# Optimization experiments

Measured on AMD Instinct MI355X. Metric: run time of the kernel, lower is better.

Reference implementation:

```python
import jax, jax.numpy as jnp
import numpy as np

D_MODEL, H, D_FF = 1024, 16, 4096
D_K = D_MODEL // H
EPS = 1e-5


def _layernorm(x, alpha, bias):
    # faithful to source: unbiased std (ddof=1), eps added to std (not var)
    mean = jnp.mean(x, axis=-1, keepdims=True)
    std = jnp.std(x, axis=-1, keepdims=True, ddof=1)
    return alpha * (x - mean) / (std + EPS) + bias


def setup_inputs() -> dict:
    key = jax.random.key(0)
    ks = jax.random.split(key, 12)
    B, S = 2, 2048
    s = 1.0 / np.sqrt(D_MODEL)
    inp = {
        "x": jax.random.normal(ks[0], (B, S, D_MODEL), dtype=jnp.float32),
        "mask": jnp.ones((B, 1, 1, S), dtype=jnp.int32),
        "wq": jax.random.normal(ks[1], (D_MODEL, D_MODEL), dtype=jnp.float32) * s,
        "wk": jax.random.normal(ks[2], (D_MODEL, D_MODEL), dtype=jnp.float32) * s,
        "wv": jax.random.normal(ks[3], (D_MODEL, D_MODEL), dtype=jnp.float32) * s,
        "wo": jax.random.normal(ks[4], (D_MODEL, D_MODEL), dtype=jnp.float32) * s,
        "w1": jax.random.normal(ks[5], (D_MODEL, D_FF), dtype=jnp.float32) * s,
        "b1": jnp.zeros((D_FF,), dtype=jnp.float32),
        "w2": jax.random.normal(ks[6], (D_FF, D_MODEL), dtype=jnp.float32) * (1.0 / np.sqrt(D_FF)),
        "b2": jnp.zeros((D_MODEL,), dtype=jnp.float32),
        "alpha1": jnp.ones((1,), dtype=jnp.float32),
        "bias1": jnp.zeros((1,), dtype=jnp.float32),
        "alpha2": jnp.ones((1,), dtype=jnp.float32),
        "bias2": jnp.zeros((1,), dtype=jnp.float32),
    }
    return inp


def reference(x, mask, wq, wk, wv, wo, w1, b1, w2, b2, alpha1, bias1, alpha2, bias2):
    B, S, _ = x.shape

    # --- sublayer 1: pre-norm self-attention + residual ---
    xn = _layernorm(x, alpha1, bias1)
    q = (xn @ wq).reshape(B, S, H, D_K).transpose(0, 2, 1, 3)  # [B,H,S,Dk]
    k = (xn @ wk).reshape(B, S, H, D_K).transpose(0, 2, 1, 3)
    v = (xn @ wv).reshape(B, S, H, D_K).transpose(0, 2, 1, 3)

    scores = jnp.einsum("bhqd,bhkd->bhqk", q, k) / np.sqrt(D_K)  # [B,H,S,S]
    scores = jnp.where(mask == 0, jnp.float32(-1e9), scores)
    attn = jax.nn.softmax(scores, axis=-1)
    ctx = jnp.einsum("bhqk,bhkd->bhqd", attn, v)
    ctx = ctx.transpose(0, 2, 1, 3).reshape(B, S, D_MODEL)
    x = x + ctx @ wo

    # --- sublayer 2: pre-norm FFN + residual ---
    xn = _layernorm(x, alpha2, bias2)
    h = jax.nn.relu(xn @ w1 + b1)
    x = x + h @ w2 + b2
    return x
```

## Files before the change

### kernel.cpp

```cpp
#include <hip/hip_runtime.h>
#include <hip/hip_bf16.h>

typedef __attribute__((ext_vector_type(8))) short bf16x8;
typedef __attribute__((ext_vector_type(4))) short short4v;
typedef __attribute__((ext_vector_type(4))) float floatx4;

#define MFMA16(A, B, C) __builtin_amdgcn_mfma_f32_16x16x32_bf16((A), (B), (C), 0, 0, 0)

__device__ inline short bf16bits(float f) {
  __hip_bfloat16 h = __float2bfloat16(f);
  return *reinterpret_cast<short*>(&h);
}
__device__ inline unsigned cvtpk(float lo, float hi) {
  unsigned r;
  asm("v_cvt_pk_bf16_f32 %0, %1, %2" : "=v"(r) : "v"(lo), "v"(hi));
  return r;
}
typedef __attribute__((address_space(3))) char lds_char;
typedef __attribute__((address_space(1))) const char glob_char;
__device__ inline void gll16(const void* g, void* l) {
  __builtin_amdgcn_global_load_lds((glob_char*)g, (lds_char*)l, 16, 0, 0);
}

__global__ __launch_bounds__(256) void transpose_f2b_kernel(
    const float* __restrict__ src, __hip_bfloat16* __restrict__ dst,
    int R, int C, int ldS) {
  __shared__ __align__(16) __hip_bfloat16 tile[64][72];
  const long r0 = (long)blockIdx.y * 64, c0 = (long)blockIdx.x * 64;
  for (int i = threadIdx.x; i < 1024; i += 256) {
    int r = i >> 4, c4 = (i & 15) * 4;
    float4 f = *(const float4*)&src[(r0 + r) * ldS + c0 + c4];
    short4v s;
    s[0] = bf16bits(f.x); s[1] = bf16bits(f.y);
    s[2] = bf16bits(f.z); s[3] = bf16bits(f.w);
    *(short4v*)&tile[r][c4] = s;
  }
  __syncthreads();
  for (int i = threadIdx.x; i < 512; i += 256) {
    int c = i >> 3, r8 = (i & 7) * 8;
    bf16x8 sv;
#pragma unroll
    for (int j = 0; j < 8; j++) sv[j] = *reinterpret_cast<const short*>(&tile[r8 + j][c]);
    *(bf16x8*)&dst[(c0 + c) * R + r0 + r8] = sv;
  }
}

__global__ __launch_bounds__(256) void transpose_qkv_kernel(
    const float* __restrict__ wq, const float* __restrict__ wk,
    const float* __restrict__ wv, __hip_bfloat16* __restrict__ wqkvT) {
  __shared__ __align__(16) __hip_bfloat16 tile[64][72];
  const int which = blockIdx.y >> 4;
  const float* src = which == 0 ? wq : (which == 1 ? wk : wv);
  __hip_bfloat16* dst = wqkvT + (size_t)which * 1024 * 1024;
  const long r0 = (long)(blockIdx.y & 15) * 64, c0 = (long)blockIdx.x * 64;
  for (int i = threadIdx.x; i < 1024; i += 256) {
    int r = i >> 4, c4 = (i & 15) * 4;
    float4 f = *(const float4*)&src[(r0 + r) * 1024 + c0 + c4];
    short4v s;
    s[0] = bf16bits(f.x); s[1] = bf16bits(f.y);
    s[2] = bf16bits(f.z); s[3] = bf16bits(f.w);
    *(short4v*)&tile[r][c4] = s;
  }
  __syncthreads();
  for (int i = threadIdx.x; i < 512; i += 256) {
    int c = i >> 3, r8 = (i & 7) * 8;
    bf16x8 sv;
#pragma unroll
    for (int j = 0; j < 8; j++) sv[j] = *reinterpret_cast<const short*>(&tile[r8 + j][c]);
    *(bf16x8*)&dst[(c0 + c) * 1024 + r0 + r8] = sv;
  }
}

__global__ __launch_bounds__(256) void vtrans_kernel(
    const __hip_bfloat16* __restrict__ qkv, __hip_bfloat16* __restrict__ vt) {
  __shared__ __align__(16) __hip_bfloat16 tile[64][72];
  const int bh = blockIdx.y, b = bh >> 4, h = bh & 15;
  const long s0 = (long)blockIdx.x * 64;
  const __hip_bfloat16* src = qkv + ((long)b * 2048 + s0) * 3072 + 2048 + h * 64;
  for (int i = threadIdx.x; i < 512; i += 256) {
    int s = i >> 3, d8 = (i & 7) * 8;
    *(uint4*)&tile[s][d8] = *(const uint4*)&src[(long)s * 3072 + d8];
  }
  __syncthreads();
  __hip_bfloat16* dstb = vt + (long)bh * 64 * 2048 + s0;
  for (int i = threadIdx.x; i < 512; i += 256) {
    int d = i >> 3, s8 = (i & 7) * 8;
    bf16x8 sv;
#pragma unroll
    for (int j = 0; j < 8; j++) sv[j] = *reinterpret_cast<const short*>(&tile[s8 + j][d]);
    *(bf16x8*)&dstb[(long)d * 2048 + s8] = sv;
  }
}

__global__ __launch_bounds__(256) void mask2add_kernel(
    const int* __restrict__ mask, float* __restrict__ addm,
    int* __restrict__ flags) {
  const int i = blockIdx.x * 256 + threadIdx.x;
  const int mv = mask[i];
  addm[i] = mv ? 0.f : -1e30f;
  __shared__ int ok[4];
  const unsigned long long bal = __ballot(mv != 0);
  if ((threadIdx.x & 63) == 0) ok[threadIdx.x >> 6] = (bal == ~0ull) ? 1 : 0;
  __syncthreads();
  if (threadIdx.x == 0) flags[blockIdx.x] = ok[0] & ok[1] & ok[2] & ok[3];
}

__global__ __launch_bounds__(256) void bias_add_kernel(
    const float* __restrict__ x1, const float* __restrict__ b2,
    float* __restrict__ out) {
  const int i = (blockIdx.x * 256 + threadIdx.x) * 4;
  float4 v = *(const float4*)&x1[i];
  const float4 bb = *(const float4*)&b2[i & 1023];
  v.x += bb.x; v.y += bb.y; v.z += bb.z; v.w += bb.w;
  *(float4*)&out[i] = v;
}

__global__ __launch_bounds__(256) void ln_kernel(
    const float* __restrict__ x, __hip_bfloat16* __restrict__ y,
    const float* __restrict__ alpha_p, const float* __restrict__ bias_p) {
  __shared__ float sred[8];
  const long row = blockIdx.x;
  const int t = threadIdx.x;
  const float* xr = x + row * 1024;
  float v[4];
#pragma unroll
  for (int i = 0; i < 4; i++) v[i] = xr[t * 4 + i];
  float sum = 0.f, sq = 0.f;
#pragma unroll
  for (int i = 0; i < 4; i++) { sum += v[i]; sq += v[i] * v[i]; }
#pragma unroll
  for (int off = 32; off; off >>= 1) {
    sum += __shfl_down(sum, off);
    sq += __shfl_down(sq, off);
  }
  if ((t & 63) == 0) { sred[(t >> 6) * 2] = sum; sred[(t >> 6) * 2 + 1] = sq; }
  __syncthreads();
  sum = sred[0] + sred[2] + sred[4] + sred[6];
  sq = sred[1] + sred[3] + sred[5] + sred[7];
  const float mean = sum * (1.f / 1024.f);
  float var = (sq - 1024.f * mean * mean) * (1.f / 1023.f);
  var = fmaxf(var, 0.f);
  const float denom = sqrtf(var) + 1e-5f;
  const float sc = alpha_p[0] / denom;
  const float beta = bias_p[0];
  __hip_bfloat16* yr = y + row * 1024;
#pragma unroll
  for (int i = 0; i < 4; i++) yr[t * 4 + i] = __float2bfloat16((v[i] - mean) * sc + beta);
}

template <int EPI>
__global__ __launch_bounds__(256) void gemm_bt_kernel(
    const __hip_bfloat16* __restrict__ A, const __hip_bfloat16* __restrict__ Bt,
    void* __restrict__ Cv, const float* __restrict__ bias,
    const float* __restrict__ res, int M, int N, int K) {
  __shared__ __align__(16) __hip_bfloat16 lA[2][128 * 32];
  __shared__ __align__(16) __hip_bfloat16 lB[2][128 * 32];
  const int tid = threadIdx.x;
  const int wave = tid >> 6, lane = tid & 63;
  const int quad = lane >> 4, l16 = lane & 15;
  const int wm = wave >> 1, wn = wave & 1;

  const int gx = gridDim.x;
  const int nwg = gx * gridDim.y;
  int bid = blockIdx.y * gx + blockIdx.x;
  bid = (bid & 7) * (nwg >> 3) + (bid >> 3);
  const long m0 = (long)(bid / gx) * 128;
  const long n0 = (long)(bid % gx) * 128;

  const int rA0 = tid >> 2, cA0 = (tid & 3) * 8;
  const int rA1 = (tid + 256) >> 2, cA1 = ((tid + 256) & 3) * 8;

  floatx4 acc[4][4];
#pragma unroll
  for (int i = 0; i < 4; i++)
#pragma unroll
    for (int j = 0; j < 4; j++) acc[i][j] = (floatx4){0.f, 0.f, 0.f, 0.f};

  const __hip_bfloat16* Ab = A + m0 * K;
  const __hip_bfloat16* Bb = Bt + n0 * K;

  gll16(&Ab[(long)rA0 * K + cA0], &lA[0][wave * 512]);
  gll16(&Ab[(long)rA1 * K + cA1], &lA[0][2048 + wave * 512]);
  gll16(&Bb[(long)rA0 * K + cA0], &lB[0][wave * 512]);
  gll16(&Bb[(long)rA1 * K + cA1], &lB[0][2048 + wave * 512]);

  int cur = 0;
  for (int k0 = 0; k0 < K; k0 += 32) {
    __syncthreads();
    if (k0 + 32 < K) {
      const int nxt = cur ^ 1;
      gll16(&Ab[(long)rA0 * K + k0 + 32 + cA0], &lA[nxt][wave * 512]);
      gll16(&Ab[(long)rA1 * K + k0 + 32 + cA1], &lA[nxt][2048 + wave * 512]);
      gll16(&Bb[(long)rA0 * K + k0 + 32 + cA0], &lB[nxt][wave * 512]);
      gll16(&Bb[(long)rA1 * K + k0 + 32 + cA1], &lB[nxt][2048 + wave * 512]);
    }
    bf16x8 af[4], bfr[4];
#pragma unroll
    for (int mi = 0; mi < 4; mi++)
      af[mi] = *(const bf16x8*)&lA[cur][(wm * 64 + mi * 16 + l16) * 32 + quad * 8];
#pragma unroll
    for (int ni = 0; ni < 4; ni++)
      bfr[ni] = *(const bf16x8*)&lB[cur][(wn * 64 + ni * 16 + l16) * 32 + quad * 8];
#pragma unroll
    for (int mi = 0; mi < 4; mi++)
#pragma unroll
      for (int ni = 0; ni < 4; ni++)
        acc[mi][ni] = MFMA16(af[mi], bfr[ni], acc[mi][ni]);
    cur ^= 1;
  }

#pragma unroll
  for (int mi = 0; mi < 4; mi++) {
#pragma unroll
    for (int ni = 0; ni < 4; ni++) {
#pragma unroll
      for (int r = 0; r < 4; r++) {
        const long row = m0 + wm * 64 + mi * 16 + quad * 4 + r;
        const long col = n0 + wn * 64 + ni * 16 + l16;
        const long idx = row * N + col;
        float v = acc[mi][ni][r];
        if (EPI == 0) {
          ((__hip_bfloat16*)Cv)[idx] = __float2bfloat16(v);
        } else if (EPI == 1) {
          ((float*)Cv)[idx] = v + res[idx];
        } else if (EPI == 2) {
          v += bias[col];
          ((__hip_bfloat16*)Cv)[idx] = __float2bfloat16(fmaxf(v, 0.f));
        } else if (EPI == 3) {
          float* Cf = (float*)Cv;
          Cf[idx] = Cf[idx] + v;
        }
      }
    }
  }
}

template <int EPI>
__global__ __launch_bounds__(256) void gemm64_bt_kernel(
    const __hip_bfloat16* __restrict__ A, const __hip_bfloat16* __restrict__ Bt,
    void* __restrict__ Cv, const float* __restrict__ bias,
    const float* __restrict__ res, int M, int N, int K) {
  __shared__ __align__(16) __hip_bfloat16 lA[2][128 * 32];
  __shared__ __align__(16) __hip_bfloat16 lB[2][64 * 32];
  const int tid = threadIdx.x;
  const int wave = tid >> 6, lane = tid & 63;
  const int quad = lane >> 4, l16 = lane & 15;
  const int wm = wave >> 1, wn = wave & 1;

  const int gx = gridDim.x;
  const int nwg = gx * gridDim.y;
  int bid = blockIdx.y * gx + blockIdx.x;
  bid = (bid & 7) * (nwg >> 3) + (bid >> 3);
  const long m0 = (long)(bid / gx) * 128;
  const long n0 = (long)(bid % gx) * 64;

  const int rA0 = tid >> 2, cA0 = (tid & 3) * 8;
  const int rA1 = (tid + 256) >> 2, cA1 = ((tid + 256) & 3) * 8;

  floatx4 acc[4][2];
#pragma unroll
  for (int i = 0; i < 4; i++)
#pragma unroll
    for (int j = 0; j < 2; j++) acc[i][j] = (floatx4){0.f, 0.f, 0.f, 0.f};

  const __hip_bfloat16* Ab = A + m0 * K;
  const __hip_bfloat16* Bb = Bt + n0 * K;

  gll16(&Ab[(long)rA0 * K + cA0], &lA[0][wave * 512]);
  gll16(&Ab[(long)rA1 * K + cA1], &lA[0][2048 + wave * 512]);
  gll16(&Bb[(long)rA0 * K + cA0], &lB[0][wave * 512]);

  int cur = 0;
  for (int k0 = 0; k0 < K; k0 += 32) {
    __syncthreads();
    if (k0 + 32 < K) {
      const int nxt = cur ^ 1;
      gll16(&Ab[(long)rA0 * K + k0 + 32 + cA0], &lA[nxt][wave * 512]);
      gll16(&Ab[(long)rA1 * K + k0 + 32 + cA1], &lA[nxt][2048 + wave * 512]);
      gll16(&Bb[(long)rA0 * K + k0 + 32 + cA0], &lB[nxt][wave * 512]);
    }
    bf16x8 af[4], bfr[2];
#pragma unroll
    for (int mi = 0; mi < 4; mi++)
      af[mi] = *(const bf16x8*)&lA[cur][(wm * 64 + mi * 16 + l16) * 32 + quad * 8];
#pragma unroll
    for (int ni = 0; ni < 2; ni++)
      bfr[ni] = *(const bf16x8*)&lB[cur][(wn * 32 + ni * 16 + l16) * 32 + quad * 8];
#pragma unroll
    for (int mi = 0; mi < 4; mi++)
#pragma unroll
      for (int ni = 0; ni < 2; ni++)
        acc[mi][ni] = MFMA16(af[mi], bfr[ni], acc[mi][ni]);
    cur ^= 1;
  }

#pragma unroll
  for (int mi = 0; mi < 4; mi++) {
#pragma unroll
    for (int ni = 0; ni < 2; ni++) {
#pragma unroll
      for (int r = 0; r < 4; r++) {
        const long row = m0 + wm * 64 + mi * 16 + quad * 4 + r;
        const long col = n0 + wn * 32 + ni * 16 + l16;
        const long idx = row * N + col;
        float v = acc[mi][ni][r];
        if (EPI == 1) {
          ((float*)Cv)[idx] = v + res[idx];
        } else if (EPI == 3) {
          float* Cf = (float*)Cv;
          Cf[idx] = Cf[idx] + v;
        }
      }
    }
  }
}

__global__ __launch_bounds__(256) void attn_kernel(
    const __hip_bfloat16* __restrict__ qkv, const __hip_bfloat16* __restrict__ vt,
    const float* __restrict__ addm, const int* __restrict__ flags,
    __hip_bfloat16* __restrict__ ctx) {
  __shared__ __align__(16) __hip_bfloat16 lK[2][64 * 64];
  __shared__ __align__(16) __hip_bfloat16 lV[2][64 * 64];
  const int tid = threadIdx.x, wave = tid >> 6, lane = tid & 63;
  const int quad = lane >> 4, l16 = lane & 15;
  const int bh = blockIdx.y, b = bh >> 4, h = bh & 15;
  const int q0 = blockIdx.x * 64 + wave * 16;
  const float cs = 0.18033688011112042f;
  const float inv_cs = 5.545177444479562f;

  const __hip_bfloat16* kb = qkv + (long)b * 2048 * 3072 + 1024 + h * 64;
  const __hip_bfloat16* vb = vt + (long)bh * 64 * 2048;
  const float* am = addm + b * 2048;

  int fm = 1;
#pragma unroll
  for (int i = 0; i < 8; ++i) fm &= flags[b * 8 + i];
  const bool fast = (fm != 0);

  const long qoff = ((long)b * 2048 + q0 + l16) * 3072 + h * 64;
  const bf16x8 bq0 = *(const bf16x8*)&qkv[qoff + quad * 8];
  const bf16x8 bq1 = *(const bf16x8*)&qkv[qoff + 32 + quad * 8];

  const int srow = lane >> 3;
  const int cslot = lane & 7;
  const int cg = cslot ^ srow;
  const int rbase = wave * 16 + srow;

  floatx4 o[4];
#pragma unroll
  for (int mi = 0; mi < 4; mi++) o[mi] = (floatx4){0.f, 0.f, 0.f, 0.f};
  float mrow = 10.0f, lrow = 0.f;

#pragma unroll
  for (int j = 0; j < 2; ++j) {
    const int rloc = rbase + j * 8;
    gll16(kb + (long)rloc * 3072 + cg * 8, &lK[0][(wave * 16 + j * 8) * 64]);
    gll16(vb + (long)rloc * 2048 + cg * 8, &lV[0][(wave * 16 + j * 8) * 64]);
  }

  int cur = 0;
  for (int t = 0; t < 32; ++t) {
    __syncthreads();
    if (t + 1 < 32) {
      const int nxt = cur ^ 1;
#pragma unroll
      for (int j = 0; j < 2; ++j) {
        const int rloc = rbase + j * 8;
        gll16(kb + (long)((t + 1) * 64 + rloc) * 3072 + cg * 8,
              &lK[nxt][(wave * 16 + j * 8) * 64]);
        gll16(vb + (long)rloc * 2048 + (t + 1) * 64 + cg * 8,
              &lV[nxt][(wave * 16 + j * 8) * 64]);
      }
    }
    const __hip_bfloat16* lKc = lK[cur];
    const __hip_bfloat16* lVc = lV[cur];

    floatx4 c[4];
    __builtin_amdgcn_s_setprio(1);
#pragma unroll
    for (int g = 0; g < 4; ++g) {
      const bf16x8 a0 =
          *(const bf16x8*)&lKc[(g * 16 + l16) * 64 + ((quad) ^ (l16 & 7)) * 8];
      const bf16x8 a1 =
          *(const bf16x8*)&lKc[(g * 16 + l16) * 64 + ((4 + quad) ^ (l16 & 7)) * 8];
      floatx4 cc = {0.f, 0.f, 0.f, 0.f};
      cc = MFMA16(a0, bq0, cc);
      cc = MFMA16(a1, bq1, cc);
      c[g] = cc;
    }
    __builtin_amdgcn_s_setprio(0);

    if (!fast) {
#pragma unroll
      for (int g = 0; g < 4; ++g) {
        const float4 a4 = *(const float4*)&am[t * 64 + g * 16 + quad * 4];
        c[g][0] = fmaf(a4.x, inv_cs, c[g][0]);
        c[g][1] = fmaf(a4.y, inv_cs, c[g][1]);
        c[g][2] = fmaf(a4.z, inv_cs, c[g][2]);
        c[g][3] = fmaf(a4.w, inv_cs, c[g][3]);
      }
    }

    const float mneg = -mrow;
    float p[4][4];
#pragma unroll
    for (int g = 0; g < 4; ++g)
#pragma unroll
      for (int r = 0; r < 4; ++r)
        p[g][r] = __builtin_amdgcn_exp2f(fmaf(c[g][r], cs, mneg));

    const float m0 = fmaxf(fmaxf(c[0][0], c[0][1]), c[0][2]);
    const float m1 = fmaxf(fmaxf(c[0][3], c[1][0]), c[1][1]);
    const float m2 = fmaxf(fmaxf(c[1][2], c[1][3]), c[2][0]);
    const float m3 = fmaxf(fmaxf(c[2][1], c[2][2]), c[2][3]);
    const float m4 = fmaxf(fmaxf(c[3][0], c[3][1]), c[3][2]);
    float tm = fmaxf(fmaxf(fmaxf(m0, m1), fmaxf(m2, m3)), fmaxf(m4, c[3][3]));
    tm = fmaxf(tm, __shfl_xor(tm, 16));
    tm = fmaxf(tm, __shfl_xor(tm, 32));
    const float tms = tm * cs;

    const float s0 = (p[0][0] + p[0][1]) + (p[0][2] + p[0][3]);
    const float s1 = (p[1][0] + p[1][1]) + (p[1][2] + p[1][3]);
    const float s2 = (p[2][0] + p[2][1]) + (p[2][2] + p[2][3]);
    const float s3 = (p[3][0] + p[3][1]) + (p[3][2] + p[3][3]);
    float rs = (s0 + s1) + (s2 + s3);
    rs += __shfl_xor(rs, 16);
    rs += __shfl_xor(rs, 32);

    unsigned dw[4][2];
#pragma unroll
    for (int g = 0; g < 4; ++g) {
      dw[g][0] = cvtpk(p[g][0], p[g][1]);
      dw[g][1] = cvtpk(p[g][2], p[g][3]);
    }
    const int qs0 = (quad & 1) * 2;
    const int src0 = l16 + 16 * qs0, src1 = src0 + 16;
    const bool hig = (quad >> 1) != 0;
#pragma unroll
    for (int ss = 0; ss < 2; ++ss) {
      const unsigned a0 = __shfl((int)dw[2 * ss][0], src0);
      const unsigned b0 = __shfl((int)dw[2 * ss + 1][0], src0);
      const unsigned a1 = __shfl((int)dw[2 * ss][1], src0);
      const unsigned b1 = __shfl((int)dw[2 * ss + 1][1], src0);
      const unsigned a2 = __shfl((int)dw[2 * ss][0], src1);
      const unsigned b2 = __shfl((int)dw[2 * ss + 1][0], src1);
      const unsigned a3 = __shfl((int)dw[2 * ss][1], src1);
      const unsigned b3 = __shfl((int)dw[2 * ss + 1][1], src1);
      uint4 du;
      du.x = hig ? b0 : a0;
      du.y = hig ? b1 : a1;
      du.z = hig ? b2 : a2;
      du.w = hig ? b3 : a3;
      const bf16x8 bp = *reinterpret_cast<bf16x8*>(&du);
      __builtin_amdgcn_s_setprio(1);
#pragma unroll
      for (int mi = 0; mi < 4; ++mi) {
        const bf16x8 av = *(const bf16x8*)&lVc[(mi * 16 + l16) * 64 +
                                               ((ss * 4 + quad) ^ (l16 & 7)) * 8];
        o[mi] = MFMA16(av, bp, o[mi]);
      }
      __builtin_amdgcn_s_setprio(0);
    }

    lrow += rs;
    if (__any(tms > mrow + 8.f)) {
      const float mnew = fmaxf(mrow, tms);
      const float alpha = __builtin_amdgcn_exp2f(mrow - mnew);
      mrow = mnew;
      lrow *= alpha;
#pragma unroll
      for (int mi = 0; mi < 4; mi++) o[mi] *= alpha;
    }
    cur ^= 1;
  }

  const float inv_l = 1.f / lrow;
  const long cb = ((long)b * 2048 + q0 + l16) * 1024 + h * 64;
#pragma unroll
  for (int mi = 0; mi < 4; mi++) {
    uint2 st;
    st.x = cvtpk(o[mi][0] * inv_l, o[mi][1] * inv_l);
    st.y = cvtpk(o[mi][2] * inv_l, o[mi][3] * inv_l);
    *(uint2*)&ctx[cb + mi * 16 + quad * 4] = st;
  }
}

extern "C" void kernel_launch(void* const* d_in, const int* in_sizes, int n_in,
                              void* d_out, int out_size, void* d_ws, size_t ws_size,
                              hipStream_t stream) {
  const float* x = (const float*)d_in[0];
  const int* mask = (const int*)d_in[1];
  const float* wq = (const float*)d_in[2];
  const float* wk = (const float*)d_in[3];
  const float* wv = (const float*)d_in[4];
  const float* wo = (const float*)d_in[5];
  const float* w1 = (const float*)d_in[6];
  const float* b1 = (const float*)d_in[7];
  const float* w2 = (const float*)d_in[8];
  const float* b2 = (const float*)d_in[9];
  const float* alpha1 = (const float*)d_in[10];
  const float* bias1 = (const float*)d_in[11];
  const float* alpha2 = (const float*)d_in[12];
  const float* bias2 = (const float*)d_in[13];

  char* ws = (char*)d_ws;
  char* dob = (char*)d_out;
  const size_t MiB = 1048576;
  __hip_bfloat16* qkv   = (__hip_bfloat16*)(ws + 0);
  __hip_bfloat16* wqkvT = (__hip_bfloat16*)(ws + 24 * MiB);
  __hip_bfloat16* vtb   = (__hip_bfloat16*)(ws + 24 * MiB);
  float*          x1    = (float*)(ws + 0);
  __hip_bfloat16* hc    = (__hip_bfloat16*)(ws + 16 * MiB);
  __hip_bfloat16* xn    = (__hip_bfloat16*)d_out;
  __hip_bfloat16* ctxb  = (__hip_bfloat16*)d_out;
  __hip_bfloat16* xn2   = (__hip_bfloat16*)d_out;
  __hip_bfloat16* woT   = (__hip_bfloat16*)(dob + 8 * MiB);
  __hip_bfloat16* w1Th  = (__hip_bfloat16*)(dob + 8 * MiB);
  __hip_bfloat16* w2Th  = (__hip_bfloat16*)(dob + 12 * MiB);
  float*          addm  = (float*)(dob + 12 * MiB);
  int*            flags = (int*)(dob + 12 * MiB + 16 * 1024);

  const dim3 b256(256);
  const dim3 g1k(16, 16);
  transpose_qkv_kernel<<<dim3(16, 48), b256, 0, stream>>>(wq, wk, wv, wqkvT);
  ln_kernel<<<4096, b256, 0, stream>>>(x, xn, alpha1, bias1);
  gemm_bt_kernel<0><<<dim3(24, 32), b256, 0, stream>>>(xn, wqkvT, qkv, nullptr, nullptr,
                                                       4096, 3072, 1024);
  vtrans_kernel<<<dim3(32, 32), b256, 0, stream>>>(qkv, vtb);
  mask2add_kernel<<<16, b256, 0, stream>>>(mask, addm, flags);
  attn_kernel<<<dim3(32, 32), b256, 0, stream>>>(qkv, vtb, addm, flags, ctxb);
  transpose_f2b_kernel<<<g1k, b256, 0, stream>>>(wo, woT, 1024, 1024, 1024);
  gemm64_bt_kernel<1><<<dim3(16, 32), b256, 0, stream>>>(ctxb, woT, x1, nullptr, x,
                                                         4096, 1024, 1024);
  ln_kernel<<<4096, b256, 0, stream>>>(x1, xn2, alpha2, bias2);
  for (int c = 0; c < 2; ++c) {
    transpose_f2b_kernel<<<dim3(32, 16), b256, 0, stream>>>(w1 + c * 2048, w1Th,
                                                            1024, 2048, 4096);
    gemm_bt_kernel<2><<<dim3(16, 32), b256, 0, stream>>>(xn2, w1Th, hc, b1 + c * 2048,
                                                         nullptr, 4096, 2048, 1024);
    transpose_f2b_kernel<<<dim3(16, 32), b256, 0, stream>>>(w2 + (size_t)c * 2048 * 1024,
                                                            w2Th, 2048, 1024, 1024);
    gemm64_bt_kernel<3><<<dim3(16, 32), b256, 0, stream>>>(hc, w2Th, x1, nullptr,
                                                           nullptr, 4096, 1024, 2048);
  }
  bias_add_kernel<<<4096, b256, 0, stream>>>(x1, b2, (float*)d_out);
}
```

Baseline: 438.2 us.

## Deepen gemm64 K-tile to 64 with XOR-swizzled LDS and merge prep launches

The 128x64 GEMM used for the Wo and W2 projections now stages 64-wide K slices instead of 32. It stores them in LDS with an XOR swizzle on the 16-byte chunk index, which halves the number of barrier-separated iterations and aims to avoid LDS bank conflicts on fragment reads. The V transpose, Wo transpose and mask conversion are merged into one prep kernel, and the W1 and W2 per-chunk transposes are merged into one wtrans kernel, cutting several small launches. The larger tiles double LDS use per block, which may lower occupancy.

```diff
diff --git a/kernel.cpp b/kernel.cpp
--- a/kernel.cpp
+++ b/kernel.cpp
@@ -20,29 +20,6 @@
 typedef __attribute__((address_space(1))) const char glob_char;
 __device__ inline void gll16(const void* g, void* l) {
   __builtin_amdgcn_global_load_lds((glob_char*)g, (lds_char*)l, 16, 0, 0);
-}
-
-__global__ __launch_bounds__(256) void transpose_f2b_kernel(
-    const float* __restrict__ src, __hip_bfloat16* __restrict__ dst,
-    int R, int C, int ldS) {
-  __shared__ __align__(16) __hip_bfloat16 tile[64][72];
-  const long r0 = (long)blockIdx.y * 64, c0 = (long)blockIdx.x * 64;
-  for (int i = threadIdx.x; i < 1024; i += 256) {
-    int r = i >> 4, c4 = (i & 15) * 4;
-    float4 f = *(const float4*)&src[(r0 + r) * ldS + c0 + c4];
-    short4v s;
-    s[0] = bf16bits(f.x); s[1] = bf16bits(f.y);
-    s[2] = bf16bits(f.z); s[3] = bf16bits(f.w);
-    *(short4v*)&tile[r][c4] = s;
-  }
-  __syncthreads();
-  for (int i = threadIdx.x; i < 512; i += 256) {
-    int c = i >> 3, r8 = (i & 7) * 8;
-    bf16x8 sv;
-#pragma unroll
-    for (int j = 0; j < 8; j++) sv[j] = *reinterpret_cast<const short*>(&tile[r8 + j][c]);
-    *(bf16x8*)&dst[(c0 + c) * R + r0 + r8] = sv;
-  }
 }
 
 __global__ __launch_bounds__(256) void transpose_qkv_kernel(
@@ -71,38 +48,94 @@
   }
 }
 
-__global__ __launch_bounds__(256) void vtrans_kernel(
-    const __hip_bfloat16* __restrict__ qkv, __hip_bfloat16* __restrict__ vt) {
-  __shared__ __align__(16) __hip_bfloat16 tile[64][72];
-  const int bh = blockIdx.y, b = bh >> 4, h = bh & 15;
-  const long s0 = (long)blockIdx.x * 64;
-  const __hip_bfloat16* src = qkv + ((long)b * 2048 + s0) * 3072 + 2048 + h * 64;
-  for (int i = threadIdx.x; i < 512; i += 256) {
-    int s = i >> 3, d8 = (i & 7) * 8;
-    *(uint4*)&tile[s][d8] = *(const uint4*)&src[(long)s * 3072 + d8];
-  }
-  __syncthreads();
-  __hip_bfloat16* dstb = vt + (long)bh * 64 * 2048 + s0;
-  for (int i = threadIdx.x; i < 512; i += 256) {
-    int d = i >> 3, s8 = (i & 7) * 8;
-    bf16x8 sv;
-#pragma unroll
-    for (int j = 0; j < 8; j++) sv[j] = *reinterpret_cast<const short*>(&tile[s8 + j][d]);
-    *(bf16x8*)&dstb[(long)d * 2048 + s8] = sv;
-  }
-}
-
-__global__ __launch_bounds__(256) void mask2add_kernel(
+__global__ __launch_bounds__(256) void prep_kernel(
+    const __hip_bfloat16* __restrict__ qkv, __hip_bfloat16* __restrict__ vt,
+    const float* __restrict__ wo, __hip_bfloat16* __restrict__ woT,
     const int* __restrict__ mask, float* __restrict__ addm,
     int* __restrict__ flags) {
-  const int i = blockIdx.x * 256 + threadIdx.x;
-  const int mv = mask[i];
-  addm[i] = mv ? 0.f : -1e30f;
+  __shared__ __align__(16) __hip_bfloat16 tile[64][72];
   __shared__ int ok[4];
-  const unsigned long long bal = __ballot(mv != 0);
-  if ((threadIdx.x & 63) == 0) ok[threadIdx.x >> 6] = (bal == ~0ull) ? 1 : 0;
+  const int bid = blockIdx.x;
+  if (bid < 1024) {
+    const int bh = bid >> 5, b = bh >> 4, h = bh & 15;
+    const long s0 = (long)(bid & 31) * 64;
+    const __hip_bfloat16* src = qkv + ((long)b * 2048 + s0) * 3072 + 2048 + h * 64;
+    for (int i = threadIdx.x; i < 512; i += 256) {
+      int s = i >> 3, d8 = (i & 7) * 8;
+      *(uint4*)&tile[s][d8] = *(const uint4*)&src[(long)s * 3072 + d8];
+    }
+    __syncthreads();
+    __hip_bfloat16* dstb = vt + (long)bh * 64 * 2048 + s0;
+    for (int i = threadIdx.x; i < 512; i += 256) {
+      int d = i >> 3, s8 = (i & 7) * 8;
+      bf16x8 sv;
+#pragma unroll
+      for (int j = 0; j < 8; j++) sv[j] = *reinterpret_cast<const short*>(&tile[s8 + j][d]);
+      *(bf16x8*)&dstb[(long)d * 2048 + s8] = sv;
+    }
+  } else if (bid < 1280) {
+    const int t = bid - 1024;
+    const long r0 = (long)(t >> 4) * 64, c0 = (long)(t & 15) * 64;
+    for (int i = threadIdx.x; i < 1024; i += 256) {
+      int r = i >> 4, c4 = (i & 15) * 4;
+      float4 f = *(const float4*)&wo[(r0 + r) * 1024 + c0 + c4];
+      short4v s;
+      s[0] = bf16bits(f.x); s[1] = bf16bits(f.y);
+      s[2] = bf16bits(f.z); s[3] = bf16bits(f.w);
+      *(short4v*)&tile[r][c4] = s;
+    }
+    __syncthreads();
+    for (int i = threadIdx.x; i < 512; i += 256) {
+      int c = i >> 3, r8 = (i & 7) * 8;
+      bf16x8 sv;
+#pragma unroll
+      for (int j = 0; j < 8; j++) sv[j] = *reinterpret_cast<const short*>(&tile[r8 + j][c]);
+      *(bf16x8*)&woT[(c0 + c) * 1024 + r0 + r8] = sv;
+    }
+  } else {
+    const int i = (bid - 1280) * 256 + threadIdx.x;
+    const int mv = mask[i];
+    addm[i] = mv ? 0.f : -1e30f;
+    const unsigned long long bal = __ballot(mv != 0);
+    if ((threadIdx.x & 63) == 0) ok[threadIdx.x >> 6] = (bal == ~0ull) ? 1 : 0;
+    __syncthreads();
+    if (threadIdx.x == 0) flags[bid - 1280] = ok[0] & ok[1] & ok[2] & ok[3];
+  }
+}
+
+__global__ __launch_bounds__(256) void wtrans_kernel(
+    const float* __restrict__ w1c, const float* __restrict__ w2c,
+    __hip_bfloat16* __restrict__ w1Th, __hip_bfloat16* __restrict__ w2Th) {
+  __shared__ __align__(16) __hip_bfloat16 tile[64][72];
+  const int bid = blockIdx.x;
+  const float* src;
+  __hip_bfloat16* dst;
+  int R, ldS;
+  long r0, c0;
+  if (bid < 512) {
+    src = w1c; dst = w1Th; R = 1024; ldS = 4096;
+    r0 = (long)(bid >> 5) * 64; c0 = (long)(bid & 31) * 64;
+  } else {
+    const int t = bid - 512;
+    src = w2c; dst = w2Th; R = 2048; ldS = 1024;
+    r0 = (long)(t >> 4) * 64; c0 = (long)(t & 15) * 64;
+  }
+  for (int i = threadIdx.x; i < 1024; i += 256) {
+    int r = i >> 4, c4 = (i & 15) * 4;
+    float4 f = *(const float4*)&src[(r0 + r) * ldS + c0 + c4];
+    short4v s;
+    s[0] = bf16bits(f.x); s[1] = bf16bits(f.y);
+    s[2] = bf16bits(f.z); s[3] = bf16bits(f.w);
+    *(short4v*)&tile[r][c4] = s;
+  }
   __syncthreads();
-  if (threadIdx.x == 0) flags[blockIdx.x] = ok[0] & ok[1] & ok[2] & ok[3];
+  for (int i = threadIdx.x; i < 512; i += 256) {
+    int c = i >> 3, r8 = (i & 7) * 8;
+    bf16x8 sv;
+#pragma unroll
+    for (int j = 0; j < 8; j++) sv[j] = *reinterpret_cast<const short*>(&tile[r8 + j][c]);
+    *(bf16x8*)&dst[(c0 + c) * R + r0 + r8] = sv;
+  }
 }
 
 __global__ __launch_bounds__(256) void bias_add_kernel(
@@ -240,8 +273,8 @@
     const __hip_bfloat16* __restrict__ A, const __hip_bfloat16* __restrict__ Bt,
     void* __restrict__ Cv, const float* __restrict__ bias,
     const float* __restrict__ res, int M, int N, int K) {
-  __shared__ __align__(16) __hip_bfloat16 lA[2][128 * 32];
-  __shared__ __align__(16) __hip_bfloat16 lB[2][64 * 32];
+  __shared__ __align__(16) __hip_bfloat16 lA[2][128 * 64];
+  __shared__ __align__(16) __hip_bfloat16 lB[2][64 * 64];
   const int tid = threadIdx.x;
   const int wave = tid >> 6, lane = tid & 63;
   const int quad = lane >> 4, l16 = lane & 15;
@@ -254,8 +287,8 @@
   const long m0 = (long)(bid / gx) * 128;
   const long n0 = (long)(bid % gx) * 64;
 
-  const int rA0 = tid >> 2, cA0 = (tid & 3) * 8;
-  const int rA1 = (tid + 256) >> 2, cA1 = ((tid + 256) & 3) * 8;
+  const int srow = lane >> 3;
+  const int cg = (lane & 7) ^ srow;
 
   floatx4 acc[4][2];
 #pragma unroll
@@ -266,31 +299,54 @@
   const __hip_bfloat16* Ab = A + m0 * K;
   const __hip_bfloat16* Bb = Bt + n0 * K;
 
-  gll16(&Ab[(long)rA0 * K + cA0], &lA[0][wave * 512]);
-  gll16(&Ab[(long)rA1 * K + cA1], &lA[0][2048 + wave * 512]);
-  gll16(&Bb[(long)rA0 * K + cA0], &lB[0][wave * 512]);
+#pragma unroll
+  for (int j = 0; j < 4; ++j) {
+    const int c = wave + j * 4;
+    gll16(&Ab[(long)(c * 8 + srow) * K + cg * 8], &lA[0][c * 512]);
+  }
+#pragma unroll
+  for (int j = 0; j < 2; ++j) {
+    const int c = wave + j * 4;
+    gll16(&Bb[(long)(c * 8 + srow) * K + cg * 8], &lB[0][c * 512]);
+  }
 
   int cur = 0;
-  for (int k0 = 0; k0 < K; k0 += 32) {
+  for (int k0 = 0; k0 < K; k0 += 64) {
     __syncthreads();
-    if (k0 + 32 < K) {
+    if (k0 + 64 < K) {
       const int nxt = cur ^ 1;
-      gll16(&Ab[(long)rA0 * K + k0 + 32 + cA0], &lA[nxt][wave * 512]);
-      gll16(&Ab[(long)rA1 * K + k0 + 32 + cA1], &lA[nxt][2048 + wave * 512]);
-      gll16(&Bb[(long)rA0 * K + k0 + 32 + cA0], &lB[nxt][wave * 512]);
-    }
-    bf16x8 af[4], bfr[2];
-#pragma unroll
-    for (int mi = 0; mi < 4; mi++)
-      af[mi] = *(const bf16x8*)&lA[cur][(wm * 64 + mi * 16 + l16) * 32 + quad * 8];
-#pragma unroll
-    for (int ni = 0; ni < 2; ni++)
-      bfr[ni] = *(const bf16x8*)&lB[cur][(wn * 32 + ni * 16 + l16) * 32 + quad * 8];
-#pragma unroll
-    for (int mi = 0; mi < 4; mi++)
-#pragma unroll
-      for (int ni = 0; ni < 2; ni++)
-        acc[mi][ni] = MFMA16(af[mi], bfr[ni], acc[mi][ni]);
+#pragma unroll
+      for (int j = 0; j < 4; ++j) {
+        const int c = wave + j * 4;
+        gll16(&Ab[(long)(c * 8 + srow) * K + k0 + 64 + cg * 8], &lA[nxt][c * 512]);
+      }
+#pragma unroll
+      for (int j = 0; j < 2; ++j) {
+        const int c = wave + j * 4;
+        gll16(&Bb[(long)(c * 8 + srow) * K + k0 + 64 + cg * 8], &lB[nxt][c * 512]);
+      }
+    }
+#pragma unroll
+    for (int ks = 0; ks < 2; ++ks) {
+      bf16x8 af[4], bfr[2];
+#pragma unroll
+      for (int mi = 0; mi < 4; mi++) {
+        const int row = wm * 64 + mi * 16 + l16;
+        af[mi] = *(const bf16x8*)&lA[cur][row * 64 +
+                                          (((ks * 4 + quad) ^ (l16 & 7)) * 8)];
+      }
+#pragma unroll
+      for (int ni = 0; ni < 2; ni++) {
+        const int row = wn * 32 + ni * 16 + l16;
+        bfr[ni] = *(const bf16x8*)&lB[cur][row * 64 +
+                                           (((ks * 4 + quad) ^ (l16 & 7)) * 8)];
+      }
+#pragma unroll
+      for (int mi = 0; mi < 4; mi++)
+#pragma unroll
+        for (int ni = 0; ni < 2; ni++)
+          acc[mi][ni] = MFMA16(af[mi], bfr[ni], acc[mi][ni]);
+    }
     cur ^= 1;
   }
 
@@ -521,25 +577,21 @@
   int*            flags = (int*)(dob + 12 * MiB + 16 * 1024);
 
   const dim3 b256(256);
-  const dim3 g1k(16, 16);
   transpose_qkv_kernel<<<dim3(16, 48), b256, 0, stream>>>(wq, wk, wv, wqkvT);
   ln_kernel<<<4096, b256, 0, stream>>>(x, xn, alpha1, bias1);
   gemm_bt_kernel<0><<<dim3(24, 32), b256, 0, stream>>>(xn, wqkvT, qkv, nullptr, nullptr,
                                                        4096, 3072, 1024);
-  vtrans_kernel<<<dim3(32, 32), b256, 0, stream>>>(qkv, vtb);
-  mask2add_kernel<<<16, b256, 0, stream>>>(mask, addm, flags);
+  prep_kernel<<<1296, b256, 0, stream>>>(qkv, vtb, wo, woT, mask, addm, flags);
   attn_kernel<<<dim3(32, 32), b256, 0, stream>>>(qkv, vtb, addm, flags, ctxb);
-  transpose_f2b_kernel<<<g1k, b256, 0, stream>>>(wo, woT, 1024, 1024, 1024);
   gemm64_bt_kernel<1><<<dim3(16, 32), b256, 0, stream>>>(ctxb, woT, x1, nullptr, x,
                                                          4096, 1024, 1024);
   ln_kernel<<<4096, b256, 0, stream>>>(x1, xn2, alpha2, bias2);
   for (int c = 0; c < 2; ++c) {
-    transpose_f2b_kernel<<<dim3(32, 16), b256, 0, stream>>>(w1 + c * 2048, w1Th,
-                                                            1024, 2048, 4096);
+    wtrans_kernel<<<1024, b256, 0, stream>>>(w1 + c * 2048,
+                                             w2 + (size_t)c * 2048 * 1024,
+                                             w1Th, w2Th);
     gemm_bt_kernel<2><<<dim3(16, 32), b256, 0, stream>>>(xn2, w1Th, hc, b1 + c * 2048,
                                                          nullptr, 4096, 2048, 1024);
-    transpose_f2b_kernel<<<dim3(16, 32), b256, 0, stream>>>(w2 + (size_t)c * 2048 * 1024,
-                                                            w2Th, 2048, 1024, 1024);
     gemm64_bt_kernel<3><<<dim3(16, 32), b256, 0, stream>>>(hc, w2Th, x1, nullptr,
                                                            nullptr, 4096, 1024, 2048);
   }
```

Measured after the change: 405.6 us. -7.4%, faster.
